# Kernel optimization log

Measured on AMD Instinct MI355X. Metric: run time of the kernel, lower is better.

## Reference

```python
import jax, jax.numpy as jnp
import numpy as np

N_EMBED = 512
HEAD_SIZE = 64

def setup_inputs() -> dict:
    key = jax.random.key(0)
    k1, k2, k3, k4 = jax.random.split(key, 4)
    B, T, C, H = 4, 4096, N_EMBED, HEAD_SIZE
    x = jax.random.normal(k1, (B, T, C), dtype=jnp.float32)
    # nn.Linear(C, H, bias=False): weight shape [H, C]; y = x @ W.T
    scale = 1.0 / np.sqrt(C)
    Wq = jax.random.uniform(k2, (H, C), dtype=jnp.float32, minval=-scale, maxval=scale)
    Wk = jax.random.uniform(k3, (H, C), dtype=jnp.float32, minval=-scale, maxval=scale)
    Wv = jax.random.uniform(k4, (H, C), dtype=jnp.float32, minval=-scale, maxval=scale)
    return {"x": x, "Wq": Wq, "Wk": Wk, "Wv": Wv}

def reference(x, Wq, Wk, Wv) -> jnp.ndarray:
    B, T, C = x.shape
    q = jnp.einsum('btc,hc->bth', x, Wq)   # [B,T,H]
    k = jnp.einsum('btc,hc->bth', x, Wk)
    v = jnp.einsum('btc,hc->bth', x, Wv)
    # NOTE: original scales by n_embed**-0.5 (C), not head_size**-0.5
    wei = jnp.einsum('bth,bsh->bts', q, k) * (C ** -0.5)  # [B,T,T]
    causal = jnp.tril(jnp.ones((T, T), dtype=bool))
    wei = jnp.where(causal, wei, -jnp.inf)
    wei = jax.nn.softmax(wei, axis=-1)
    out = jnp.einsum('bts,bsh->bth', wei, v)  # [B,T,H]
    return out
```

## Files before the change

kernel.cpp:

```cpp
#include <hip/hip_runtime.h>

typedef float f32x4 __attribute__((ext_vector_type(4)));
typedef __bf16 bf16x8 __attribute__((ext_vector_type(8)));
typedef __bf16 bf16x4 __attribute__((ext_vector_type(4)));
typedef short short4v __attribute__((ext_vector_type(4)));

#define MFMA32K(a, b, c) __builtin_amdgcn_mfma_f32_16x16x32_bf16((a), (b), (c), 0, 0, 0)
#define MFMA16K(a, b, c) __builtin_amdgcn_mfma_f32_16x16x16bf16_1k((a), (b), (c), 0, 0, 0)
#define CFENCE() asm volatile("" ::: "memory")
#define DSFENCE() asm volatile("s_waitcnt lgkmcnt(0)" ::: "memory")

constexpr int Tn = 4096, Cn = 512, Hn = 64;
constexpr float QSCALE = 1.4426950408889634f * 0.04419417382415922f;
constexpr float M0 = -30000.0f;

__global__ void wconv(const float* __restrict__ Wq, const float* __restrict__ Wk,
                      const float* __restrict__ Wv, __bf16* __restrict__ Wb) {
    int t = blockIdx.y;
    int i = blockIdx.x * 256 + threadIdx.x;
    const float* src = (t == 0) ? Wq : (t == 1) ? Wk : Wv;
    float scale = (t == 0) ? QSCALE : 1.0f;
    Wb[t * Hn * Cn + i] = (__bf16)(src[i] * scale);
}

__device__ inline bf16x8 cvt8(float4 u0, float4 u1) {
    bf16x8 r;
    r[0] = (__bf16)u0.x; r[1] = (__bf16)u0.y; r[2] = (__bf16)u0.z; r[3] = (__bf16)u0.w;
    r[4] = (__bf16)u1.x; r[5] = (__bf16)u1.y; r[6] = (__bf16)u1.z; r[7] = (__bf16)u1.w;
    return r;
}

__global__ __launch_bounds__(256) void proj(const float* __restrict__ x,
                                            const __bf16* __restrict__ Wb,
                                            __bf16* __restrict__ Qb,
                                            __bf16* __restrict__ Kb,
                                            __bf16* __restrict__ VF) {
    const int tid = threadIdx.x;
    const int lane = tid & 63, wid = tid >> 6;
    const int c = lane & 15, h = lane >> 4;
    const int row0 = blockIdx.x * 64 + wid * 16;

    __shared__ __bf16 Ws[2][192 * 36];
    __shared__ __bf16 tb[4][16][72];

    f32x4 acc[3][4] = {};
    const float* xr = x + (size_t)(row0 + c) * Cn;

#pragma unroll
    for (int i = 0; i < 3; ++i) {
        int g = tid + i * 256, r = g >> 2, gc = g & 3;
        *(bf16x8*)&Ws[0][r * 36 + gc * 8] = *(const bf16x8*)(Wb + (size_t)r * Cn + gc * 8);
    }
    float4 xc0 = *(const float4*)(xr + 8 * h);
    float4 xc1 = *(const float4*)(xr + 8 * h + 4);
    __syncthreads();

#pragma unroll 2
    for (int ks = 0; ks < 16; ++ks) {
        const int cur = ks & 1;
        bf16x8 wreg[3];
        float4 xn0, xn1;
        if (ks < 15) {
#pragma unroll
            for (int i = 0; i < 3; ++i) {
                int g = tid + i * 256, r = g >> 2, gc = g & 3;
                wreg[i] = *(const bf16x8*)(Wb + (size_t)r * Cn + (ks + 1) * 32 + gc * 8);
            }
            xn0 = *(const float4*)(xr + (ks + 1) * 32 + 8 * h);
            xn1 = *(const float4*)(xr + (ks + 1) * 32 + 8 * h + 4);
        }
        bf16x8 a0 = cvt8(xc0, xc1);
#pragma unroll
        for (int w = 0; w < 3; ++w)
#pragma unroll
            for (int nt = 0; nt < 4; ++nt) {
                bf16x8 bf = *(const bf16x8*)&Ws[cur][(w * 64 + nt * 16 + c) * 36 + 8 * h];
                acc[w][nt] = MFMA32K(a0, bf, acc[w][nt]);
            }
        if (ks < 15) {
#pragma unroll
            for (int i = 0; i < 3; ++i) {
                int g = tid + i * 256, r = g >> 2, gc = g & 3;
                *(bf16x8*)&Ws[cur ^ 1][r * 36 + gc * 8] = wreg[i];
            }
            xc0 = xn0; xc1 = xn1;
        }
        __syncthreads();
    }

#pragma unroll
    for (int w = 0; w < 2; ++w) {
        CFENCE();
#pragma unroll
        for (int nt = 0; nt < 4; ++nt)
#pragma unroll
            for (int r = 0; r < 4; ++r)
                tb[wid][h * 4 + r][nt * 16 + c] = (__bf16)acc[w][nt][r];
        DSFENCE();
        __bf16* dst = (w == 0) ? Qb : Kb;
#pragma unroll
        for (int ch = 0; ch < 2; ++ch) {
            int rr = ch * 8 + (lane >> 3);
            bf16x8 vv = *(const bf16x8*)(&tb[wid][rr][(lane & 7) * 8]);
            *(bf16x8*)(dst + (size_t)(row0 + rr) * Hn + (lane & 7) * 8) = vv;
        }
        CFENCE();
    }

    const int b = row0 >> 12;
    const int t0 = row0 & (Tn - 1);
    const int tile = t0 >> 4;
#pragma unroll
    for (int nt = 0; nt < 4; ++nt) {
        f32x4 a = acc[2][nt];
        bf16x4 v4;
        v4[0] = (__bf16)a.x; v4[1] = (__bf16)a.y;
        v4[2] = (__bf16)a.z; v4[3] = (__bf16)a.w;
        size_t off = ((size_t)((b * 256 + tile) * 4 + h) * 64 + (nt * 16 + c)) * 4;
        *(bf16x4*)(VF + off) = v4;
    }
}

__global__ __launch_bounds__(512) void attn(const __bf16* __restrict__ Qb,
                                            const __bf16* __restrict__ Kb,
                                            const __bf16* __restrict__ VF,
                                            float* __restrict__ out) {
    const int tid = threadIdx.x;
    const int lane = tid & 63, ks = tid >> 6;
    const int c = lane & 15, h = lane >> 4;
    const int g = 63 - (int)(blockIdx.x >> 2);
    const int b = blockIdx.x & 3;
    const int qbase = g * 64;

    const __bf16* Kbase = Kb + (size_t)b * Tn * Hn;
    const __bf16* Vbase = VF + (size_t)b * 256 * 1024;

    bf16x8 qf[4][2];
#pragma unroll
    for (int qs = 0; qs < 4; ++qs) {
        const __bf16* qp = Qb + (size_t)(b * Tn + qbase + qs * 16 + c) * Hn;
        qf[qs][0] = *(const bf16x8*)(qp + 8 * h);
        qf[qs][1] = *(const bf16x8*)(qp + 32 + 8 * h);
    }

    f32x4 o[4][4] = {};
    float m[4] = {M0, M0, M0, M0};
    float l[4] = {};

    const int nkv = g + 1;

    for (int kt = ks; kt < nkv; kt += 8) {
        const int j0 = kt * 64;
        short4v vf[4][4];
        const __bf16* vt = Vbase + ((size_t)(j0 >> 4) << 10) + (h << 8);
#pragma unroll
        for (int dt = 0; dt < 4; ++dt)
#pragma unroll
            for (int ct = 0; ct < 4; ++ct)
                vf[dt][ct] = *(const short4v*)(vt + (ct << 10) + ((dt * 16 + c) << 2));
        bf16x8 kf[4][2];
#pragma unroll
        for (int ct = 0; ct < 4; ++ct) {
            const __bf16* kp = Kbase + (size_t)(j0 + ct * 16 + c) * Hn;
            kf[ct][0] = *(const bf16x8*)(kp + 8 * h);
            kf[ct][1] = *(const bf16x8*)(kp + 32 + 8 * h);
        }
        const bool diag = (kt == g);

#pragma unroll
        for (int qs = 0; qs < 4; ++qs) {
            f32x4 s[4];
#pragma unroll
            for (int ct = 0; ct < 4; ++ct) {
                f32x4 z = {};
                z = MFMA32K(kf[ct][0], qf[qs][0], z);
                z = MFMA32K(kf[ct][1], qf[qs][1], z);
                s[ct] = z;
            }
            if (diag) {
#pragma unroll
                for (int ct = 0; ct < 4; ++ct)
#pragma unroll
                    for (int r = 0; r < 4; ++r)
                        if (j0 + ct * 16 + 4 * h + r > qbase + qs * 16 + c)
                            s[ct][r] = -1e30f;
            }
            float lm = fmaxf(fmaxf(fmaxf(s[0][0], s[0][1]), fmaxf(s[0][2], s[0][3])),
                             fmaxf(fmaxf(s[1][0], s[1][1]), fmaxf(s[1][2], s[1][3])));
            lm = fmaxf(lm, fmaxf(fmaxf(fmaxf(s[2][0], s[2][1]), fmaxf(s[2][2], s[2][3])),
                                 fmaxf(fmaxf(s[3][0], s[3][1]), fmaxf(s[3][2], s[3][3]))));
            if (!__all(lm <= m[qs] + 8.0f)) {
                float rm = fmaxf(lm, __shfl_xor(lm, 16));
                rm = fmaxf(rm, __shfl_xor(rm, 32));
                float mn = fmaxf(m[qs], rm);
                float sc = __builtin_amdgcn_exp2f(m[qs] - mn);
                m[qs] = mn;
                l[qs] *= sc;
#pragma unroll
                for (int dt = 0; dt < 4; ++dt) o[qs][dt] *= sc;
            }
            short4v pf[4];
            float lsum = 0.0f;
#pragma unroll
            for (int ct = 0; ct < 4; ++ct) {
                bf16x4 pb;
#pragma unroll
                for (int r = 0; r < 4; ++r) {
                    float p = __builtin_amdgcn_exp2f(s[ct][r] - m[qs]);
                    lsum += p;
                    pb[r] = (__bf16)p;
                }
                pf[ct] = __builtin_bit_cast(short4v, pb);
            }
            l[qs] += lsum;
#pragma unroll
            for (int dt = 0; dt < 4; ++dt)
#pragma unroll
                for (int ct = 0; ct < 4; ++ct)
                    o[qs][dt] = MFMA16K(vf[dt][ct], pf[ct], o[qs][dt]);
        }
    }

#pragma unroll
    for (int qs = 0; qs < 4; ++qs) {
        l[qs] += __shfl_xor(l[qs], 16);
        l[qs] += __shfl_xor(l[qs], 32);
    }

    __shared__ float Mo[4][64][68];
    __shared__ float Mml[4][64][8];
#pragma unroll
    for (int step = 4; step >= 1; step >>= 1) {
        if (ks >= step && ks < 2 * step) {
            int slot = ks - step;
#pragma unroll
            for (int qs = 0; qs < 4; ++qs) {
                Mml[slot][lane][qs] = m[qs];
                Mml[slot][lane][4 + qs] = l[qs];
#pragma unroll
                for (int dt = 0; dt < 4; ++dt)
                    *(f32x4*)&Mo[slot][lane][(qs * 4 + dt) * 4] = o[qs][dt];
            }
        }
        __syncthreads();
        if (ks < step) {
#pragma unroll
            for (int qs = 0; qs < 4; ++qs) {
                float m2 = Mml[ks][lane][qs];
                float l2 = Mml[ks][lane][4 + qs];
                float M = fmaxf(m[qs], m2);
                float e1 = __builtin_amdgcn_exp2f(m[qs] - M);
                float e2 = __builtin_amdgcn_exp2f(m2 - M);
                m[qs] = M;
                l[qs] = l[qs] * e1 + l2 * e2;
#pragma unroll
                for (int dt = 0; dt < 4; ++dt) {
                    f32x4 o2 = *(const f32x4*)&Mo[ks][lane][(qs * 4 + dt) * 4];
                    o[qs][dt] = o[qs][dt] * e1 + o2 * e2;
                }
            }
        }
        __syncthreads();
    }

    if (ks == 0) {
#pragma unroll
        for (int qs = 0; qs < 4; ++qs) {
            float rl = 1.0f / l[qs];
            float* ob = out + ((size_t)(b * Tn + qbase + qs * 16 + c)) * Hn;
#pragma unroll
            for (int dt = 0; dt < 4; ++dt) {
                f32x4 v = o[qs][dt] * rl;
                *(f32x4*)(ob + dt * 16 + 4 * h) = v;
            }
        }
    }
}

extern "C" void kernel_launch(void* const* d_in, const int* in_sizes, int n_in,
                              void* d_out, int out_size, void* d_ws, size_t ws_size,
                              hipStream_t stream) {
    const float* x  = (const float*)d_in[0];
    const float* Wq = (const float*)d_in[1];
    const float* Wk = (const float*)d_in[2];
    const float* Wv = (const float*)d_in[3];
    float* out = (float*)d_out;

    char* ws = (char*)d_ws;
    __bf16* Wb = (__bf16*)ws;
    __bf16* Qb = (__bf16*)(ws + 196608);
    __bf16* Kb = (__bf16*)(ws + 196608 + 2097152);
    __bf16* VF = (__bf16*)(ws + 196608 + 2 * 2097152);

    wconv<<<dim3(128, 3), 256, 0, stream>>>(Wq, Wk, Wv, Wb);
    proj<<<256, 256, 0, stream>>>(x, Wb, Qb, Kb, VF);
    attn<<<256, 512, 0, stream>>>(Qb, Kb, VF, out);
}
```

Before: 55.65 us.

## Fuse weight conversion, projection and attention into one cooperative kernel

Merges the three kernels (weight bf16 conversion, QKV projection, causal attention) into a single cooperative launch separated by grid-wide syncs, removing two kernel launch gaps. The projection is restructured to use 512 threads with split-K across wave pairs reduced through shared memory, and it reads weights directly from global memory instead of double-buffering them in LDS. Shared memory is unioned between phases. The grid syncs add their own cost, and the direct global weight reads may be slower than the LDS staging.

New measurement: 134.6 us. 142% more time.

```diff
diff --git a/kernel.cpp b/kernel.cpp
--- a/kernel.cpp
+++ b/kernel.cpp
@@ -1,4 +1,7 @@
 #include <hip/hip_runtime.h>
+#include <hip/hip_cooperative_groups.h>
+
+namespace cg = cooperative_groups;
 
 typedef float f32x4 __attribute__((ext_vector_type(4)));
 typedef __bf16 bf16x8 __attribute__((ext_vector_type(8)));
@@ -14,14 +17,15 @@
 constexpr float QSCALE = 1.4426950408889634f * 0.04419417382415922f;
 constexpr float M0 = -30000.0f;
 
-__global__ void wconv(const float* __restrict__ Wq, const float* __restrict__ Wk,
-                      const float* __restrict__ Wv, __bf16* __restrict__ Wb) {
-    int t = blockIdx.y;
-    int i = blockIdx.x * 256 + threadIdx.x;
-    const float* src = (t == 0) ? Wq : (t == 1) ? Wk : Wv;
-    float scale = (t == 0) ? QSCALE : 1.0f;
-    Wb[t * Hn * Cn + i] = (__bf16)(src[i] * scale);
-}
+struct SmemA {
+    float ml[4][64][52];
+    __bf16 tb[4][16][72];
+};
+struct SmemB {
+    float Mo[4][64][68];
+    float Mml[4][64][8];
+};
+union Smem { SmemA a; SmemB b; };
 
 __device__ inline bf16x8 cvt8(float4 u0, float4 u1) {
     bf16x8 r;
@@ -30,248 +34,246 @@
     return r;
 }
 
-__global__ __launch_bounds__(256) void proj(const float* __restrict__ x,
-                                            const __bf16* __restrict__ Wb,
-                                            __bf16* __restrict__ Qb,
-                                            __bf16* __restrict__ Kb,
-                                            __bf16* __restrict__ VF) {
+__global__ __launch_bounds__(512, 2) void fused(
+        const float* __restrict__ x, const float* __restrict__ Wq,
+        const float* __restrict__ Wk, const float* __restrict__ Wv,
+        __bf16* __restrict__ Wb, __bf16* __restrict__ Qb,
+        __bf16* __restrict__ Kb, __bf16* __restrict__ VF,
+        float* __restrict__ out) {
+    __shared__ Smem sm;
     const int tid = threadIdx.x;
+    const int bid = blockIdx.x;
     const int lane = tid & 63, wid = tid >> 6;
     const int c = lane & 15, h = lane >> 4;
-    const int row0 = blockIdx.x * 64 + wid * 16;
-
-    __shared__ __bf16 Ws[2][192 * 36];
-    __shared__ __bf16 tb[4][16][72];
-
-    f32x4 acc[3][4] = {};
-    const float* xr = x + (size_t)(row0 + c) * Cn;
-
-#pragma unroll
-    for (int i = 0; i < 3; ++i) {
-        int g = tid + i * 256, r = g >> 2, gc = g & 3;
-        *(bf16x8*)&Ws[0][r * 36 + gc * 8] = *(const bf16x8*)(Wb + (size_t)r * Cn + gc * 8);
+
+    {
+        int i = bid * 512 + tid;
+        if (i < 3 * Hn * Cn) {
+            int t = i / (Hn * Cn);
+            int r = i - t * (Hn * Cn);
+            const float* src = (t == 0) ? Wq : (t == 1) ? Wk : Wv;
+            float scale = (t == 0) ? QSCALE : 1.0f;
+            Wb[i] = (__bf16)(src[r] * scale);
+        }
     }
-    float4 xc0 = *(const float4*)(xr + 8 * h);
-    float4 xc1 = *(const float4*)(xr + 8 * h + 4);
-    __syncthreads();
-
-#pragma unroll 2
-    for (int ks = 0; ks < 16; ++ks) {
-        const int cur = ks & 1;
-        bf16x8 wreg[3];
-        float4 xn0, xn1;
-        if (ks < 15) {
-#pragma unroll
-            for (int i = 0; i < 3; ++i) {
-                int g = tid + i * 256, r = g >> 2, gc = g & 3;
-                wreg[i] = *(const bf16x8*)(Wb + (size_t)r * Cn + (ks + 1) * 32 + gc * 8);
-            }
-            xn0 = *(const float4*)(xr + (ks + 1) * 32 + 8 * h);
-            xn1 = *(const float4*)(xr + (ks + 1) * 32 + 8 * h + 4);
-        }
-        bf16x8 a0 = cvt8(xc0, xc1);
-#pragma unroll
-        for (int w = 0; w < 3; ++w)
+    cg::this_grid().sync();
+
+    {
+        const int rg = wid >> 1, kh = wid & 1;
+        const int row0 = bid * 64 + rg * 16;
+
+        f32x4 acc[3][4] = {};
+        const float* xr = x + (size_t)(row0 + c) * Cn + kh * 256;
+
+#pragma unroll
+        for (int ks = 0; ks < 8; ++ks) {
+            const int kb = ks * 32 + 8 * h;
+            const float4* p0 = (const float4*)(xr + kb);
+            bf16x8 a0 = cvt8(p0[0], p0[1]);
+#pragma unroll
+            for (int w = 0; w < 3; ++w)
+#pragma unroll
+                for (int nt = 0; nt < 4; ++nt) {
+                    bf16x8 bf = *(const bf16x8*)(Wb + (size_t)(w * Hn + nt * 16 + c) * Cn + kh * 256 + kb);
+                    acc[w][nt] = MFMA32K(a0, bf, acc[w][nt]);
+                }
+        }
+
+        if (kh) {
+#pragma unroll
+            for (int w = 0; w < 3; ++w)
+#pragma unroll
+                for (int nt = 0; nt < 4; ++nt)
+                    *(f32x4*)&sm.a.ml[rg][lane][(w * 4 + nt) * 4] = acc[w][nt];
+        }
+        __syncthreads();
+        if (!kh) {
+#pragma unroll
+            for (int w = 0; w < 3; ++w)
+#pragma unroll
+                for (int nt = 0; nt < 4; ++nt)
+                    acc[w][nt] += *(const f32x4*)&sm.a.ml[rg][lane][(w * 4 + nt) * 4];
+
+#pragma unroll
+            for (int w = 0; w < 2; ++w) {
+                CFENCE();
+#pragma unroll
+                for (int nt = 0; nt < 4; ++nt)
+#pragma unroll
+                    for (int r = 0; r < 4; ++r)
+                        sm.a.tb[rg][h * 4 + r][nt * 16 + c] = (__bf16)acc[w][nt][r];
+                DSFENCE();
+                __bf16* dst = (w == 0) ? Qb : Kb;
+#pragma unroll
+                for (int ch = 0; ch < 2; ++ch) {
+                    int rr = ch * 8 + (lane >> 3);
+                    bf16x8 vv = *(const bf16x8*)(&sm.a.tb[rg][rr][(lane & 7) * 8]);
+                    *(bf16x8*)(dst + (size_t)(row0 + rr) * Hn + (lane & 7) * 8) = vv;
+                }
+                CFENCE();
+            }
+
+            const int b = row0 >> 12;
+            const int t0 = row0 & (Tn - 1);
+            const int tile = t0 >> 4;
 #pragma unroll
             for (int nt = 0; nt < 4; ++nt) {
-                bf16x8 bf = *(const bf16x8*)&Ws[cur][(w * 64 + nt * 16 + c) * 36 + 8 * h];
-                acc[w][nt] = MFMA32K(a0, bf, acc[w][nt]);
-            }
-        if (ks < 15) {
-#pragma unroll
-            for (int i = 0; i < 3; ++i) {
-                int g = tid + i * 256, r = g >> 2, gc = g & 3;
-                *(bf16x8*)&Ws[cur ^ 1][r * 36 + gc * 8] = wreg[i];
-            }
-            xc0 = xn0; xc1 = xn1;
-        }
-        __syncthreads();
+                f32x4 a = acc[2][nt];
+                bf16x4 v4;
+                v4[0] = (__bf16)a.x; v4[1] = (__bf16)a.y;
+                v4[2] = (__bf16)a.z; v4[3] = (__bf16)a.w;
+                size_t off = ((size_t)((b * 256 + tile) * 4 + h) * 64 + (nt * 16 + c)) * 4;
+                *(bf16x4*)(VF + off) = v4;
+            }
+        }
     }
-
-#pragma unroll
-    for (int w = 0; w < 2; ++w) {
-        CFENCE();
-#pragma unroll
-        for (int nt = 0; nt < 4; ++nt)
-#pragma unroll
-            for (int r = 0; r < 4; ++r)
-                tb[wid][h * 4 + r][nt * 16 + c] = (__bf16)acc[w][nt][r];
-        DSFENCE();
-        __bf16* dst = (w == 0) ? Qb : Kb;
-#pragma unroll
-        for (int ch = 0; ch < 2; ++ch) {
-            int rr = ch * 8 + (lane >> 3);
-            bf16x8 vv = *(const bf16x8*)(&tb[wid][rr][(lane & 7) * 8]);
-            *(bf16x8*)(dst + (size_t)(row0 + rr) * Hn + (lane & 7) * 8) = vv;
-        }
-        CFENCE();
-    }
-
-    const int b = row0 >> 12;
-    const int t0 = row0 & (Tn - 1);
-    const int tile = t0 >> 4;
-#pragma unroll
-    for (int nt = 0; nt < 4; ++nt) {
-        f32x4 a = acc[2][nt];
-        bf16x4 v4;
-        v4[0] = (__bf16)a.x; v4[1] = (__bf16)a.y;
-        v4[2] = (__bf16)a.z; v4[3] = (__bf16)a.w;
-        size_t off = ((size_t)((b * 256 + tile) * 4 + h) * 64 + (nt * 16 + c)) * 4;
-        *(bf16x4*)(VF + off) = v4;
-    }
-}
-
-__global__ __launch_bounds__(512) void attn(const __bf16* __restrict__ Qb,
-                                            const __bf16* __restrict__ Kb,
-                                            const __bf16* __restrict__ VF,
-                                            float* __restrict__ out) {
-    const int tid = threadIdx.x;
-    const int lane = tid & 63, ks = tid >> 6;
-    const int c = lane & 15, h = lane >> 4;
-    const int g = 63 - (int)(blockIdx.x >> 2);
-    const int b = blockIdx.x & 3;
-    const int qbase = g * 64;
-
-    const __bf16* Kbase = Kb + (size_t)b * Tn * Hn;
-    const __bf16* Vbase = VF + (size_t)b * 256 * 1024;
-
-    bf16x8 qf[4][2];
-#pragma unroll
-    for (int qs = 0; qs < 4; ++qs) {
-        const __bf16* qp = Qb + (size_t)(b * Tn + qbase + qs * 16 + c) * Hn;
-        qf[qs][0] = *(const bf16x8*)(qp + 8 * h);
-        qf[qs][1] = *(const bf16x8*)(qp + 32 + 8 * h);
-    }
-
-    f32x4 o[4][4] = {};
-    float m[4] = {M0, M0, M0, M0};
-    float l[4] = {};
-
-    const int nkv = g + 1;
-
-    for (int kt = ks; kt < nkv; kt += 8) {
-        const int j0 = kt * 64;
-        short4v vf[4][4];
-        const __bf16* vt = Vbase + ((size_t)(j0 >> 4) << 10) + (h << 8);
-#pragma unroll
-        for (int dt = 0; dt < 4; ++dt)
-#pragma unroll
-            for (int ct = 0; ct < 4; ++ct)
-                vf[dt][ct] = *(const short4v*)(vt + (ct << 10) + ((dt * 16 + c) << 2));
-        bf16x8 kf[4][2];
-#pragma unroll
-        for (int ct = 0; ct < 4; ++ct) {
-            const __bf16* kp = Kbase + (size_t)(j0 + ct * 16 + c) * Hn;
-            kf[ct][0] = *(const bf16x8*)(kp + 8 * h);
-            kf[ct][1] = *(const bf16x8*)(kp + 32 + 8 * h);
-        }
-        const bool diag = (kt == g);
-
+    cg::this_grid().sync();
+
+    {
+        const int ks = wid;
+        const int g = 63 - (bid >> 2);
+        const int b = bid & 3;
+        const int qbase = g * 64;
+
+        const __bf16* Kbase = Kb + (size_t)b * Tn * Hn;
+        const __bf16* Vbase = VF + (size_t)b * 256 * 1024;
+
+        bf16x8 qf[4][2];
 #pragma unroll
         for (int qs = 0; qs < 4; ++qs) {
-            f32x4 s[4];
+            const __bf16* qp = Qb + (size_t)(b * Tn + qbase + qs * 16 + c) * Hn;
+            qf[qs][0] = *(const bf16x8*)(qp + 8 * h);
+            qf[qs][1] = *(const bf16x8*)(qp + 32 + 8 * h);
+        }
+
+        f32x4 o[4][4] = {};
+        float m[4] = {M0, M0, M0, M0};
+        float l[4] = {};
+
+        const int nkv = g + 1;
+
+        for (int kt = ks; kt < nkv; kt += 8) {
+            const int j0 = kt * 64;
+            short4v vf[4][4];
+            const __bf16* vt = Vbase + ((size_t)(j0 >> 4) << 10) + (h << 8);
+#pragma unroll
+            for (int dt = 0; dt < 4; ++dt)
+#pragma unroll
+                for (int ct = 0; ct < 4; ++ct)
+                    vf[dt][ct] = *(const short4v*)(vt + (ct << 10) + ((dt * 16 + c) << 2));
+            bf16x8 kf[4][2];
 #pragma unroll
             for (int ct = 0; ct < 4; ++ct) {
-                f32x4 z = {};
-                z = MFMA32K(kf[ct][0], qf[qs][0], z);
-                z = MFMA32K(kf[ct][1], qf[qs][1], z);
-                s[ct] = z;
-            }
-            if (diag) {
-#pragma unroll
-                for (int ct = 0; ct < 4; ++ct)
-#pragma unroll
-                    for (int r = 0; r < 4; ++r)
-                        if (j0 + ct * 16 + 4 * h + r > qbase + qs * 16 + c)
-                            s[ct][r] = -1e30f;
-            }
-            float lm = fmaxf(fmaxf(fmaxf(s[0][0], s[0][1]), fmaxf(s[0][2], s[0][3])),
-                             fmaxf(fmaxf(s[1][0], s[1][1]), fmaxf(s[1][2], s[1][3])));
-            lm = fmaxf(lm, fmaxf(fmaxf(fmaxf(s[2][0], s[2][1]), fmaxf(s[2][2], s[2][3])),
-                                 fmaxf(fmaxf(s[3][0], s[3][1]), fmaxf(s[3][2], s[3][3]))));
-            if (!__all(lm <= m[qs] + 8.0f)) {
-                float rm = fmaxf(lm, __shfl_xor(lm, 16));
-                rm = fmaxf(rm, __shfl_xor(rm, 32));
-                float mn = fmaxf(m[qs], rm);
-                float sc = __builtin_amdgcn_exp2f(m[qs] - mn);
-                m[qs] = mn;
-                l[qs] *= sc;
-#pragma unroll
-                for (int dt = 0; dt < 4; ++dt) o[qs][dt] *= sc;
-            }
-            short4v pf[4];
-            float lsum = 0.0f;
-#pragma unroll
-            for (int ct = 0; ct < 4; ++ct) {
-                bf16x4 pb;
-#pragma unroll
-                for (int r = 0; r < 4; ++r) {
-                    float p = __builtin_amdgcn_exp2f(s[ct][r] - m[qs]);
-                    lsum += p;
-                    pb[r] = (__bf16)p;
-                }
-                pf[ct] = __builtin_bit_cast(short4v, pb);
-            }
-            l[qs] += lsum;
-#pragma unroll
-            for (int dt = 0; dt < 4; ++dt)
-#pragma unroll
-                for (int ct = 0; ct < 4; ++ct)
-                    o[qs][dt] = MFMA16K(vf[dt][ct], pf[ct], o[qs][dt]);
-        }
-    }
-
-#pragma unroll
-    for (int qs = 0; qs < 4; ++qs) {
-        l[qs] += __shfl_xor(l[qs], 16);
-        l[qs] += __shfl_xor(l[qs], 32);
-    }
-
-    __shared__ float Mo[4][64][68];
-    __shared__ float Mml[4][64][8];
-#pragma unroll
-    for (int step = 4; step >= 1; step >>= 1) {
-        if (ks >= step && ks < 2 * step) {
-            int slot = ks - step;
+                const __bf16* kp = Kbase + (size_t)(j0 + ct * 16 + c) * Hn;
+                kf[ct][0] = *(const bf16x8*)(kp + 8 * h);
+                kf[ct][1] = *(const bf16x8*)(kp + 32 + 8 * h);
+            }
+            const bool diag = (kt == g);
+
 #pragma unroll
             for (int qs = 0; qs < 4; ++qs) {
-                Mml[slot][lane][qs] = m[qs];
-                Mml[slot][lane][4 + qs] = l[qs];
+                f32x4 s[4];
+#pragma unroll
+                for (int ct = 0; ct < 4; ++ct) {
+                    f32x4 z = {};
+                    z = MFMA32K(kf[ct][0], qf[qs][0], z);
+                    z = MFMA32K(kf[ct][1], qf[qs][1], z);
+                    s[ct] = z;
+                }
+                if (diag) {
+#pragma unroll
+                    for (int ct = 0; ct < 4; ++ct)
+#pragma unroll
+                        for (int r = 0; r < 4; ++r)
+                            if (j0 + ct * 16 + 4 * h + r > qbase + qs * 16 + c)
+                                s[ct][r] = -1e30f;
+                }
+                float lm = fmaxf(fmaxf(fmaxf(s[0][0], s[0][1]), fmaxf(s[0][2], s[0][3])),
+                                 fmaxf(fmaxf(s[1][0], s[1][1]), fmaxf(s[1][2], s[1][3])));
+                lm = fmaxf(lm, fmaxf(fmaxf(fmaxf(s[2][0], s[2][1]), fmaxf(s[2][2], s[2][3])),
+                                     fmaxf(fmaxf(s[3][0], s[3][1]), fmaxf(s[3][2], s[3][3]))));
+                if (!__all(lm <= m[qs] + 8.0f)) {
+                    float rm = fmaxf(lm, __shfl_xor(lm, 16));
+                    rm = fmaxf(rm, __shfl_xor(rm, 32));
+                    float mn = fmaxf(m[qs], rm);
+                    float sc = __builtin_amdgcn_exp2f(m[qs] - mn);
+                    m[qs] = mn;
+                    l[qs] *= sc;
+#pragma unroll
+                    for (int dt = 0; dt < 4; ++dt) o[qs][dt] *= sc;
+                }
+                short4v pf[4];
+                float lsum = 0.0f;
+#pragma unroll
+                for (int ct = 0; ct < 4; ++ct) {
+                    bf16x4 pb;
+#pragma unroll
+                    for (int r = 0; r < 4; ++r) {
+                        float p = __builtin_amdgcn_exp2f(s[ct][r] - m[qs]);
+                        lsum += p;
+                        pb[r] = (__bf16)p;
+                    }
+                    pf[ct] = __builtin_bit_cast(short4v, pb);
+                }
+                l[qs] += lsum;
 #pragma unroll
                 for (int dt = 0; dt < 4; ++dt)
-                    *(f32x4*)&Mo[slot][lane][(qs * 4 + dt) * 4] = o[qs][dt];
-            }
-        }
-        __syncthreads();
-        if (ks < step) {
+#pragma unroll
+                    for (int ct = 0; ct < 4; ++ct)
+                        o[qs][dt] = MFMA16K(vf[dt][ct], pf[ct], o[qs][dt]);
+            }
+        }
+
+#pragma unroll
+        for (int qs = 0; qs < 4; ++qs) {
+            l[qs] += __shfl_xor(l[qs], 16);
+            l[qs] += __shfl_xor(l[qs], 32);
+        }
+
+#pragma unroll
+        for (int step = 4; step >= 1; step >>= 1) {
+            if (ks >= step && ks < 2 * step) {
+                int slot = ks - step;
+#pragma unroll
+                for (int qs = 0; qs < 4; ++qs) {
+                    sm.b.Mml[slot][lane][qs] = m[qs];
+                    sm.b.Mml[slot][lane][4 + qs] = l[qs];
+#pragma unroll
+                    for (int dt = 0; dt < 4; ++dt)
+                        *(f32x4*)&sm.b.Mo[slot][lane][(qs * 4 + dt) * 4] = o[qs][dt];
+                }
+            }
+            __syncthreads();
+            if (ks < step) {
+#pragma unroll
+                for (int qs = 0; qs < 4; ++qs) {
+                    float m2 = sm.b.Mml[ks][lane][qs];
+                    float l2 = sm.b.Mml[ks][lane][4 + qs];
+                    float M = fmaxf(m[qs], m2);
+                    float e1 = __builtin_amdgcn_exp2f(m[qs] - M);
+                    float e2 = __builtin_amdgcn_exp2f(m2 - M);
+                    m[qs] = M;
+                    l[qs] = l[qs] * e1 + l2 * e2;
+#pragma unroll
+                    for (int dt = 0; dt < 4; ++dt) {
+                        f32x4 o2 = *(const f32x4*)&sm.b.Mo[ks][lane][(qs * 4 + dt) * 4];
+                        o[qs][dt] = o[qs][dt] * e1 + o2 * e2;
+                    }
+                }
+            }
+            __syncthreads();
+        }
+
+        if (ks == 0) {
 #pragma unroll
             for (int qs = 0; qs < 4; ++qs) {
-                float m2 = Mml[ks][lane][qs];
-                float l2 = Mml[ks][lane][4 + qs];
-                float M = fmaxf(m[qs], m2);
-                float e1 = __builtin_amdgcn_exp2f(m[qs] - M);
-                float e2 = __builtin_amdgcn_exp2f(m2 - M);
-                m[qs] = M;
-                l[qs] = l[qs] * e1 + l2 * e2;
+                float rl = 1.0f / l[qs];
+                float* ob = out + ((size_t)(b * Tn + qbase + qs * 16 + c)) * Hn;
 #pragma unroll
                 for (int dt = 0; dt < 4; ++dt) {
-                    f32x4 o2 = *(const f32x4*)&Mo[ks][lane][(qs * 4 + dt) * 4];
-                    o[qs][dt] = o[qs][dt] * e1 + o2 * e2;
-                }
-            }
-        }
-        __syncthreads();
-    }
-
-    if (ks == 0) {
-#pragma unroll
-        for (int qs = 0; qs < 4; ++qs) {
-            float rl = 1.0f / l[qs];
-            float* ob = out + ((size_t)(b * Tn + qbase + qs * 16 + c)) * Hn;
-#pragma unroll
-            for (int dt = 0; dt < 4; ++dt) {
-                f32x4 v = o[qs][dt] * rl;
-                *(f32x4*)(ob + dt * 16 + 4 * h) = v;
+                    f32x4 v = o[qs][dt] * rl;
+                    *(f32x4*)(ob + dt * 16 + 4 * h) = v;
+                }
             }
         }
     }
@@ -292,7 +294,7 @@
     __bf16* Kb = (__bf16*)(ws + 196608 + 2097152);
     __bf16* VF = (__bf16*)(ws + 196608 + 2 * 2097152);
 
-    wconv<<<dim3(128, 3), 256, 0, stream>>>(Wq, Wk, Wv, Wb);
-    proj<<<256, 256, 0, stream>>>(x, Wb, Qb, Kb, VF);
-    attn<<<256, 512, 0, stream>>>(Qb, Kb, VF, out);
+    void* args[] = {(void*)&x, (void*)&Wq, (void*)&Wk, (void*)&Wv,
+                    (void*)&Wb, (void*)&Qb, (void*)&Kb, (void*)&VF, (void*)&out};
+    hipLaunchCooperativeKernel((void*)fused, dim3(256), dim3(512), args, 0, stream);
 }
```

## Balance causal work by pairing 32-row query tiles and prefetch K tiles

Applied to the files above, without the earlier changes.

Each block now processes two 32-row query groups, v and 127-v, one after the other, instead of a single 64-row group. Pairing a short causal row range with a long one evens out the number of KV tiles per block, so the critical path is no longer set by the blocks near the end of the sequence. K fragments for the next KV tile are also loaded into registers before the current tile's compute, to hide global-load latency. The cost is a second cross-wave LDS merge and output pass per block, plus extra registers for the prefetched K fragments.

New measurement: 56.37 us. About the same (+1.3%).

```diff
diff --git a/kernel.cpp b/kernel.cpp
--- a/kernel.cpp
+++ b/kernel.cpp
@@ -128,150 +128,175 @@
     const int tid = threadIdx.x;
     const int lane = tid & 63, ks = tid >> 6;
     const int c = lane & 15, h = lane >> 4;
-    const int g = 63 - (int)(blockIdx.x >> 2);
     const int b = blockIdx.x & 3;
-    const int qbase = g * 64;
+    const int v = blockIdx.x >> 2;
 
     const __bf16* Kbase = Kb + (size_t)b * Tn * Hn;
     const __bf16* Vbase = VF + (size_t)b * 256 * 1024;
 
-    bf16x8 qf[4][2];
-#pragma unroll
-    for (int qs = 0; qs < 4; ++qs) {
-        const __bf16* qp = Qb + (size_t)(b * Tn + qbase + qs * 16 + c) * Hn;
-        qf[qs][0] = *(const bf16x8*)(qp + 8 * h);
-        qf[qs][1] = *(const bf16x8*)(qp + 32 + 8 * h);
-    }
-
-    f32x4 o[4][4] = {};
-    float m[4] = {M0, M0, M0, M0};
-    float l[4] = {};
-
-    const int nkv = g + 1;
-
-    for (int kt = ks; kt < nkv; kt += 8) {
-        const int j0 = kt * 64;
-        short4v vf[4][4];
-        const __bf16* vt = Vbase + ((size_t)(j0 >> 4) << 10) + (h << 8);
-#pragma unroll
-        for (int dt = 0; dt < 4; ++dt)
-#pragma unroll
-            for (int ct = 0; ct < 4; ++ct)
-                vf[dt][ct] = *(const short4v*)(vt + (ct << 10) + ((dt * 16 + c) << 2));
-        bf16x8 kf[4][2];
-#pragma unroll
-        for (int ct = 0; ct < 4; ++ct) {
-            const __bf16* kp = Kbase + (size_t)(j0 + ct * 16 + c) * Hn;
-            kf[ct][0] = *(const bf16x8*)(kp + 8 * h);
-            kf[ct][1] = *(const bf16x8*)(kp + 32 + 8 * h);
-        }
-        const bool diag = (kt == g);
-
-#pragma unroll
-        for (int qs = 0; qs < 4; ++qs) {
-            f32x4 s[4];
+    __shared__ float Mo[4][64][36];
+    __shared__ float Mml[4][64][4];
+
+#pragma unroll 1
+    for (int grp = 0; grp < 2; ++grp) {
+        const int vg = grp ? (127 - v) : v;
+        const int qbase = vg * 32;
+        const int nkv = vg / 2 + 1;
+
+        bf16x8 qf[2][2];
+#pragma unroll
+        for (int qs = 0; qs < 2; ++qs) {
+            const __bf16* qp = Qb + (size_t)(b * Tn + qbase + qs * 16 + c) * Hn;
+            qf[qs][0] = *(const bf16x8*)(qp + 8 * h);
+            qf[qs][1] = *(const bf16x8*)(qp + 32 + 8 * h);
+        }
+
+        f32x4 o[2][4] = {};
+        float m[2] = {M0, M0};
+        float l[2] = {};
+
+        bf16x8 kfc[4][2];
+        {
+            const int kt0 = (ks < nkv) ? ks : nkv - 1;
 #pragma unroll
             for (int ct = 0; ct < 4; ++ct) {
-                f32x4 z = {};
-                z = MFMA32K(kf[ct][0], qf[qs][0], z);
-                z = MFMA32K(kf[ct][1], qf[qs][1], z);
-                s[ct] = z;
-            }
-            if (diag) {
+                const __bf16* kp = Kbase + (size_t)(kt0 * 64 + ct * 16 + c) * Hn;
+                kfc[ct][0] = *(const bf16x8*)(kp + 8 * h);
+                kfc[ct][1] = *(const bf16x8*)(kp + 32 + 8 * h);
+            }
+        }
+
+        for (int kt = ks; kt < nkv; kt += 8) {
+            const int j0 = kt * 64;
+            bf16x8 kfn[4][2];
+            {
+                const int ktn = (kt + 8 < nkv) ? kt + 8 : kt;
+#pragma unroll
+                for (int ct = 0; ct < 4; ++ct) {
+                    const __bf16* kp = Kbase + (size_t)(ktn * 64 + ct * 16 + c) * Hn;
+                    kfn[ct][0] = *(const bf16x8*)(kp + 8 * h);
+                    kfn[ct][1] = *(const bf16x8*)(kp + 32 + 8 * h);
+                }
+            }
+            short4v vf[4][4];
+            const __bf16* vt = Vbase + ((size_t)(j0 >> 4) << 10) + (h << 8);
+#pragma unroll
+            for (int dt = 0; dt < 4; ++dt)
 #pragma unroll
                 for (int ct = 0; ct < 4; ++ct)
-#pragma unroll
-                    for (int r = 0; r < 4; ++r)
-                        if (j0 + ct * 16 + 4 * h + r > qbase + qs * 16 + c)
-                            s[ct][r] = -1e30f;
-            }
-            float lm = fmaxf(fmaxf(fmaxf(s[0][0], s[0][1]), fmaxf(s[0][2], s[0][3])),
-                             fmaxf(fmaxf(s[1][0], s[1][1]), fmaxf(s[1][2], s[1][3])));
-            lm = fmaxf(lm, fmaxf(fmaxf(fmaxf(s[2][0], s[2][1]), fmaxf(s[2][2], s[2][3])),
-                                 fmaxf(fmaxf(s[3][0], s[3][1]), fmaxf(s[3][2], s[3][3]))));
-            if (!__all(lm <= m[qs] + 8.0f)) {
-                float rm = fmaxf(lm, __shfl_xor(lm, 16));
-                rm = fmaxf(rm, __shfl_xor(rm, 32));
-                float mn = fmaxf(m[qs], rm);
-                float sc = __builtin_amdgcn_exp2f(m[qs] - mn);
-                m[qs] = mn;
-                l[qs] *= sc;
-#pragma unroll
-                for (int dt = 0; dt < 4; ++dt) o[qs][dt] *= sc;
-            }
-            short4v pf[4];
-            float lsum = 0.0f;
+                    vf[dt][ct] = *(const short4v*)(vt + (ct << 10) + ((dt * 16 + c) << 2));
+
+            const bool diag = (kt == nkv - 1);
+
+#pragma unroll
+            for (int qs = 0; qs < 2; ++qs) {
+                f32x4 s[4];
+#pragma unroll
+                for (int ct = 0; ct < 4; ++ct) {
+                    f32x4 z = {};
+                    z = MFMA32K(kfc[ct][0], qf[qs][0], z);
+                    z = MFMA32K(kfc[ct][1], qf[qs][1], z);
+                    s[ct] = z;
+                }
+                if (diag) {
+#pragma unroll
+                    for (int ct = 0; ct < 4; ++ct)
+#pragma unroll
+                        for (int r = 0; r < 4; ++r)
+                            if (j0 + ct * 16 + 4 * h + r > qbase + qs * 16 + c)
+                                s[ct][r] = -1e30f;
+                }
+                float lm = fmaxf(fmaxf(fmaxf(s[0][0], s[0][1]), fmaxf(s[0][2], s[0][3])),
+                                 fmaxf(fmaxf(s[1][0], s[1][1]), fmaxf(s[1][2], s[1][3])));
+                lm = fmaxf(lm, fmaxf(fmaxf(fmaxf(s[2][0], s[2][1]), fmaxf(s[2][2], s[2][3])),
+                                     fmaxf(fmaxf(s[3][0], s[3][1]), fmaxf(s[3][2], s[3][3]))));
+                if (!__all(lm <= m[qs] + 8.0f)) {
+                    float rm = fmaxf(lm, __shfl_xor(lm, 16));
+                    rm = fmaxf(rm, __shfl_xor(rm, 32));
+                    float mn = fmaxf(m[qs], rm);
+                    float sc = __builtin_amdgcn_exp2f(m[qs] - mn);
+                    m[qs] = mn;
+                    l[qs] *= sc;
+#pragma unroll
+                    for (int dt = 0; dt < 4; ++dt) o[qs][dt] *= sc;
+                }
+                short4v pf[4];
+                float lsum = 0.0f;
+#pragma unroll
+                for (int ct = 0; ct < 4; ++ct) {
+                    bf16x4 pb;
+#pragma unroll
+                    for (int r = 0; r < 4; ++r) {
+                        float p = __builtin_amdgcn_exp2f(s[ct][r] - m[qs]);
+                        lsum += p;
+                        pb[r] = (__bf16)p;
+                    }
+                    pf[ct] = __builtin_bit_cast(short4v, pb);
+                }
+                l[qs] += lsum;
+#pragma unroll
+                for (int dt = 0; dt < 4; ++dt)
+#pragma unroll
+                    for (int ct = 0; ct < 4; ++ct)
+                        o[qs][dt] = MFMA16K(vf[dt][ct], pf[ct], o[qs][dt]);
+            }
 #pragma unroll
             for (int ct = 0; ct < 4; ++ct) {
-                bf16x4 pb;
-#pragma unroll
-                for (int r = 0; r < 4; ++r) {
-                    float p = __builtin_amdgcn_exp2f(s[ct][r] - m[qs]);
-                    lsum += p;
-                    pb[r] = (__bf16)p;
-                }
-                pf[ct] = __builtin_bit_cast(short4v, pb);
-            }
-            l[qs] += lsum;
-#pragma unroll
-            for (int dt = 0; dt < 4; ++dt)
-#pragma unroll
-                for (int ct = 0; ct < 4; ++ct)
-                    o[qs][dt] = MFMA16K(vf[dt][ct], pf[ct], o[qs][dt]);
-        }
-    }
-
-#pragma unroll
-    for (int qs = 0; qs < 4; ++qs) {
-        l[qs] += __shfl_xor(l[qs], 16);
-        l[qs] += __shfl_xor(l[qs], 32);
-    }
-
-    __shared__ float Mo[4][64][68];
-    __shared__ float Mml[4][64][8];
-#pragma unroll
-    for (int step = 4; step >= 1; step >>= 1) {
-        if (ks >= step && ks < 2 * step) {
-            int slot = ks - step;
-#pragma unroll
-            for (int qs = 0; qs < 4; ++qs) {
-                Mml[slot][lane][qs] = m[qs];
-                Mml[slot][lane][4 + qs] = l[qs];
-#pragma unroll
-                for (int dt = 0; dt < 4; ++dt)
-                    *(f32x4*)&Mo[slot][lane][(qs * 4 + dt) * 4] = o[qs][dt];
-            }
-        }
-        __syncthreads();
-        if (ks < step) {
-#pragma unroll
-            for (int qs = 0; qs < 4; ++qs) {
-                float m2 = Mml[ks][lane][qs];
-                float l2 = Mml[ks][lane][4 + qs];
-                float M = fmaxf(m[qs], m2);
-                float e1 = __builtin_amdgcn_exp2f(m[qs] - M);
-                float e2 = __builtin_amdgcn_exp2f(m2 - M);
-                m[qs] = M;
-                l[qs] = l[qs] * e1 + l2 * e2;
+                kfc[ct][0] = kfn[ct][0];
+                kfc[ct][1] = kfn[ct][1];
+            }
+        }
+
+#pragma unroll
+        for (int qs = 0; qs < 2; ++qs) {
+            l[qs] += __shfl_xor(l[qs], 16);
+            l[qs] += __shfl_xor(l[qs], 32);
+        }
+
+#pragma unroll
+        for (int step = 4; step >= 1; step >>= 1) {
+            if (ks >= step && ks < 2 * step) {
+                int slot = ks - step;
+#pragma unroll
+                for (int qs = 0; qs < 2; ++qs) {
+                    Mml[slot][lane][qs] = m[qs];
+                    Mml[slot][lane][2 + qs] = l[qs];
+#pragma unroll
+                    for (int dt = 0; dt < 4; ++dt)
+                        *(f32x4*)&Mo[slot][lane][(qs * 4 + dt) * 4] = o[qs][dt];
+                }
+            }
+            __syncthreads();
+            if (ks < step) {
+#pragma unroll
+                for (int qs = 0; qs < 2; ++qs) {
+                    float m2 = Mml[ks][lane][qs];
+                    float l2 = Mml[ks][lane][2 + qs];
+                    float M = fmaxf(m[qs], m2);
+                    float e1 = __builtin_amdgcn_exp2f(m[qs] - M);
+                    float e2 = __builtin_amdgcn_exp2f(m2 - M);
+                    m[qs] = M;
+                    l[qs] = l[qs] * e1 + l2 * e2;
+#pragma unroll
+                    for (int dt = 0; dt < 4; ++dt) {
+                        f32x4 o2 = *(const f32x4*)&Mo[ks][lane][(qs * 4 + dt) * 4];
+                        o[qs][dt] = o[qs][dt] * e1 + o2 * e2;
+                    }
+                }
+            }
+            __syncthreads();
+        }
+
+        if (ks == 0) {
+#pragma unroll
+            for (int qs = 0; qs < 2; ++qs) {
+                float rl = 1.0f / l[qs];
+                float* ob = out + ((size_t)(b * Tn + qbase + qs * 16 + c)) * Hn;
 #pragma unroll
                 for (int dt = 0; dt < 4; ++dt) {
-                    f32x4 o2 = *(const f32x4*)&Mo[ks][lane][(qs * 4 + dt) * 4];
-                    o[qs][dt] = o[qs][dt] * e1 + o2 * e2;
-                }
-            }
-        }
-        __syncthreads();
-    }
-
-    if (ks == 0) {
-#pragma unroll
-        for (int qs = 0; qs < 4; ++qs) {
-            float rl = 1.0f / l[qs];
-            float* ob = out + ((size_t)(b * Tn + qbase + qs * 16 + c)) * Hn;
-#pragma unroll
-            for (int dt = 0; dt < 4; ++dt) {
-                f32x4 v = o[qs][dt] * rl;
-                *(f32x4*)(ob + dt * 16 + 4 * h) = v;
+                    f32x4 w = o[qs][dt] * rl;
+                    *(f32x4*)(ob + dt * 16 + 4 * h) = w;
+                }
             }
         }
     }
```
